# Performance work log

Hardware: AMD Instinct MI355X
Metric: run time of the kernel (lower is better)

The kernel has to match this reference:

```python
import jax, jax.numpy as jnp
import numpy as np

B, H, C, LB, PW = 8192, 128, 1, 64, 32
WL = LB + PW


def setup_inputs() -> dict:
    key = jax.random.key(0)
    ks = jax.random.split(key, 9)
    inv_sqrt_h = 1.0 / np.sqrt(H)
    return {
        "x": jax.random.normal(ks[0], (B, LB, 1), jnp.float32),
        # per-step Linear weights for F (hidden->hidden) and H (hidden->target)
        "F_w": jax.random.normal(ks[1], (WL, H, H), jnp.float32) * inv_sqrt_h,
        "F_b": jax.random.normal(ks[2], (WL, H), jnp.float32) * 0.05,
        "H_w": jax.random.normal(ks[3], (WL, C, H), jnp.float32) * inv_sqrt_h,
        "H_b": jax.random.normal(ks[4], (WL, C), jnp.float32) * 0.05,
        "init_state": jax.random.normal(ks[5], (H,), jnp.float32),
        # well-conditioned covariance / noise params so inv(S) is stable
        "init_cov": jnp.eye(H, dtype=jnp.float32) + 0.02 * jax.random.normal(ks[6], (H, H), jnp.float32),
        "Q": 0.1 * jnp.eye(H, dtype=jnp.float32) + 0.01 * jax.random.normal(ks[7], (H, H), jnp.float32),
        "R": 0.1 * jnp.eye(C, dtype=jnp.float32) + 0.01 * jax.random.normal(ks[8], (C, C), jnp.float32),
    }


def _kalman_forward(x, F_w, F_b, H_w, H_b, init_state, init_cov, Q, R):
    b = x.shape[0]
    h = init_state.shape[0]
    I = jnp.eye(h, dtype=x.dtype)
    hs0 = jnp.broadcast_to(init_state, (b, h))
    P0 = jnp.broadcast_to(init_cov, (b, h, h))
    obs = jnp.moveaxis(x[:, :LB, :C], 0, 1)  # (LB, B, C)

    def filt_step(carry, inp):
        hs, P = carry
        Fw, Fb, Hw, Hb, y = inp
        hs_pred = hs @ Fw.T + Fb                                   # (B, h)
        P_pred = jnp.einsum('ij,bjk,lk->bil', Fw, P, Fw) + Q       # (B, h, h)
        y_pred = hs_pred @ Hw.T + Hb                               # (B, c)
        resid = y - y_pred
        S = jnp.einsum('ij,bjk,lk->bil', Hw, P_pred, Hw) + R       # (B, c, c)
        PHt = jnp.einsum('bij,kj->bik', P_pred, Hw)                # (B, h, c)
        K = PHt @ jnp.linalg.inv(S)                                # (B, h, c)
        hs_new = hs_pred + jnp.einsum('bhc,bc->bh', K, resid)
        P_new = (I - jnp.einsum('bhc,ck->bhk', K, Hw)) @ P_pred
        return (hs_new, P_new), None

    (hs, _), _ = jax.lax.scan(
        filt_step, (hs0, P0), (F_w[:LB], F_b[:LB], H_w[:LB], H_b[:LB], obs))

    def pred_step(hs, inp):
        Fw, Fb, Hw, Hb = inp
        hs = hs @ Fw.T + Fb
        em = hs @ Hw.T + Hb                                        # (B, c)
        return hs, em

    _, ems = jax.lax.scan(pred_step, hs, (F_w[LB:], F_b[LB:], H_w[LB:], H_b[LB:]))
    # ems: (PW, B, C) -> torch.cat(dim=1) order -> (B, PW*C) -> unsqueeze(-1)
    out = jnp.moveaxis(ems, 0, 1).reshape(b, PW * C)
    return out[..., None]


def reference(x, F_w, F_b, H_w, H_b, init_state, init_cov, Q, R):
    return _kalman_forward(x, F_w, F_b, H_w, H_b, init_state, init_cov, Q, R)
```

## Files before the change

kernel.cpp:

```cpp
#include <hip/hip_runtime.h>

#define NB 8192
#define NH 128
#define NLB 64
#define NPW 32
#define MAGIC 1234567
#define SP 136

typedef __attribute__((ext_vector_type(8))) __bf16 bf16x8;
typedef __attribute__((ext_vector_type(4))) __bf16 bf16x4;
typedef __attribute__((ext_vector_type(4))) float f32x4;

__device__ __forceinline__ f32x4 mfma3(bf16x8 ah, bf16x8 al, bf16x8 bh, bf16x8 bl, f32x4 c) {
    c = __builtin_amdgcn_mfma_f32_16x16x32_bf16(ah, bh, c, 0, 0, 0);
    c = __builtin_amdgcn_mfma_f32_16x16x32_bf16(ah, bl, c, 0, 0, 0);
    c = __builtin_amdgcn_mfma_f32_16x16x32_bf16(al, bh, c, 0, 0, 0);
    return c;
}

__device__ __forceinline__ void ld_split8(const float* p, bf16x8& h, bf16x8& l) {
    float vv[8];
    *(float4*)vv       = *(const float4*)p;
    *(float4*)(vv + 4) = *(const float4*)(p + 4);
#pragma unroll
    for (int j = 0; j < 8; ++j) {
        __bf16 t = (__bf16)vv[j];
        h[j] = t;
        l[j] = (__bf16)(vv[j] - (float)t);
    }
}

#define KT_OFF   560
#define g63_OFF  (KT_OFF + 8192)
#define MR_OFF   (g63_OFF + 128)
#define DV_OFF   (MR_OFF + 2048)
#define DP_OFF   (DV_OFF + 32)
#define UV_OFF   (DP_OFF + 32)
#define SINK_OFF 32000
#define FLAG_I   34000
#define FHI_OFF  40960
#define FLO_OFF  (FHI_OFF + 524288)
#define WS_SPLIT_BYTES  ((size_t)(FLO_OFF + 524288) * 4)

#define DYN_LDS  ((144 + 144 + 128 + 128) * SP * 2)

__global__ __launch_bounds__(256)
void k0_split(const float* __restrict__ F, float* __restrict__ ws)
{
    size_t e = ((size_t)blockIdx.x * 256 + threadIdx.x) * 8;
    __bf16* fh = (__bf16*)(ws + FHI_OFF);
    __bf16* fl = (__bf16*)(ws + FLO_OFF);
    float v[8];
    *(float4*)v       = *(const float4*)(F + e);
    *(float4*)(v + 4) = *(const float4*)(F + e + 4);
    bf16x8 h, l;
#pragma unroll
    for (int j = 0; j < 8; ++j) {
        __bf16 t = (__bf16)v[j];
        h[j] = t;
        l[j] = (__bf16)(v[j] - (float)t);
    }
    *(bf16x8*)&fh[e] = h;
    *(bf16x8*)&fl[e] = l;
}

__global__ __launch_bounds__(1024) __attribute__((amdgpu_waves_per_eu(4, 4)))
void k1_recur(const float* __restrict__ Fw,
              const float* __restrict__ Fb,
              const float* __restrict__ Hw,
              const float* __restrict__ Hb,
              const float* __restrict__ init_state,
              const float* __restrict__ init_cov,
              const float* __restrict__ Qm,
              const float* __restrict__ Rm,
              float* __restrict__ ws,
              int use_split)
{
    const int tid = threadIdx.x;
    const int wg  = blockIdx.x;
    int* wsl = (int*)ws;

    extern __shared__ __align__(16) char dsm[];
    __bf16* PhiS = (__bf16*)dsm;
    __bf16* PloS = PhiS + 144 * SP;
    __bf16* UhiS = PloS + 144 * SP;
    __bf16* UloS = UhiS + 128 * SP;

    __shared__ float smisc[1280];
    __shared__ __align__(16) float shH[NH];
    __shared__ __align__(16) float shFW[NH];
    __shared__ float shK[NH], shV[NH], shFV[NH], shG[NH], shGn[NH];
    __shared__ float scal[16];

    float* pV = smisc;
    float* pW = smisc + 640;

    if (wg == 0) {
        const float Rv = Rm[0];
        const int lane = tid & 63, w = tid >> 6;
        const int lm = lane & 15, kg = lane >> 4;
        const int a = w >> 2, b = w & 3;
        const int arow = a * 32, bcol = b * 32;

#pragma unroll
        for (int ii = 0; ii < 16; ++ii) {
            int e = tid + ii * 1024;
            int r = e >> 7, c = e & 127;
            float v = init_cov[e];
            __bf16 h = (__bf16)v;
            PhiS[r * SP + c] = h;
            PloS[r * SP + c] = (__bf16)(v - (float)h);
        }
#pragma unroll
        for (int ii = 0; ii < 2; ++ii) {
            int e = tid + ii * 1024;
            int r = 128 + (e >> 7), c = e & 127;
            float v = (r == 130) ? init_state[c] : 0.f;
            __bf16 h = (__bf16)v;
            PhiS[r * SP + c] = h;
            PloS[r * SP + c] = (__bf16)(v - (float)h);
        }
        if (tid < NH) shG[tid] = init_state[tid];
        if (tid == 0) scal[1] = 0.f;

        f32x4 qreg[2][2];
#pragma unroll
        for (int rt2 = 0; rt2 < 2; ++rt2)
#pragma unroll
            for (int ct2 = 0; ct2 < 2; ++ct2)
                qreg[rt2][ct2] =
                    *(const f32x4*)&Qm[(bcol + rt2 * 16 + lm) * 128 + arow + ct2 * 16 + kg * 4];
        __syncthreads();

        for (int t = 0; t < NLB; ++t) {
            if (tid < NH) shH[tid] = Hw[t * NH + tid];
            bf16x8 fbH[2][4], fbL[2][4];
            if (use_split) {
                const __bf16* fh = (const __bf16*)(ws + FHI_OFF) + (size_t)t * 16384;
                const __bf16* fl = (const __bf16*)(ws + FLO_OFF) + (size_t)t * 16384;
#pragma unroll
                for (int rs = 0; rs < 2; ++rs)
#pragma unroll
                    for (int kc = 0; kc < 4; ++kc) {
                        int ro = (bcol + rs * 16 + lm) * 128 + kc * 32 + kg * 8;
                        fbH[rs][kc] = *(const bf16x8*)&fh[ro];
                        fbL[rs][kc] = *(const bf16x8*)&fl[ro];
                    }
            } else {
                const float* Ft = Fw + (size_t)t * 16384;
#pragma unroll
                for (int rs = 0; rs < 2; ++rs)
#pragma unroll
                    for (int kc = 0; kc < 4; ++kc)
                        ld_split8(Ft + (bcol + rs * 16 + lm) * 128 + kc * 32 + kg * 8,
                                  fbH[rs][kc], fbL[rs][kc]);
            }

            const f32x4 zero4 = {0.f, 0.f, 0.f, 0.f};
            f32x4 accU[2][2];
#pragma unroll
            for (int rt = 0; rt < 2; ++rt)
#pragma unroll
                for (int ct = 0; ct < 2; ++ct) accU[rt][ct] = zero4;
#pragma unroll
            for (int kc = 0; kc < 4; ++kc) {
#pragma unroll
                for (int rt = 0; rt < 2; ++rt) {
                    bf16x8 ph = *(bf16x8*)&PhiS[(arow + rt * 16 + lm) * SP + kc * 32 + kg * 8];
                    bf16x8 pl = *(bf16x8*)&PloS[(arow + rt * 16 + lm) * SP + kc * 32 + kg * 8];
#pragma unroll
                    for (int ct = 0; ct < 2; ++ct)
                        accU[rt][ct] = mfma3(ph, pl, fbH[ct][kc], fbL[ct][kc], accU[rt][ct]);
                }
            }
            if (a == 0) {
                f32x4 accV[2];
                accV[0] = zero4; accV[1] = zero4;
#pragma unroll
                for (int kc = 0; kc < 4; ++kc) {
                    bf16x8 vh = *(bf16x8*)&PhiS[(128 + lm) * SP + kc * 32 + kg * 8];
                    bf16x8 vl = *(bf16x8*)&PloS[(128 + lm) * SP + kc * 32 + kg * 8];
#pragma unroll
                    for (int ct = 0; ct < 2; ++ct)
                        accV[ct] = mfma3(vh, vl, fbH[ct][kc], fbL[ct][kc], accV[ct]);
                }
                if (kg == 0) {
#pragma unroll
                    for (int ct = 0; ct < 2; ++ct) {
                        int c = bcol + ct * 16 + lm;
                        shFW[c] = accV[ct][0];
                        shFV[c] = accV[ct][1];
                        shGn[c] = accV[ct][2];
                    }
                }
            }
#pragma unroll
            for (int rt = 0; rt < 2; ++rt)
#pragma unroll
                for (int ct = 0; ct < 2; ++ct) {
                    int Urow = arow + rt * 16 + kg * 4;
                    int Ucol = bcol + ct * 16 + lm;
                    bf16x4 uh, ul;
#pragma unroll
                    for (int reg = 0; reg < 4; ++reg) {
                        float v = accU[rt][ct][reg];
                        __bf16 h = (__bf16)v;
                        uh[reg] = h;
                        ul[reg] = (__bf16)(v - (float)h);
                    }
                    *(bf16x4*)&UhiS[Ucol * SP + Urow] = uh;
                    *(bf16x4*)&UloS[Ucol * SP + Urow] = ul;
                }
            __syncthreads();

            f32x4 accP[2][2];
#pragma unroll
            for (int rt2 = 0; rt2 < 2; ++rt2)
#pragma unroll
                for (int ct2 = 0; ct2 < 2; ++ct2) accP[rt2][ct2] = qreg[rt2][ct2];
#pragma unroll
            for (int kc = 0; kc < 4; ++kc) {
#pragma unroll
                for (int ct2 = 0; ct2 < 2; ++ct2) {
                    bf16x8 uh = *(bf16x8*)&UhiS[(arow + ct2 * 16 + lm) * SP + kc * 32 + kg * 8];
                    bf16x8 ul = *(bf16x8*)&UloS[(arow + ct2 * 16 + lm) * SP + kc * 32 + kg * 8];
#pragma unroll
                    for (int rt2 = 0; rt2 < 2; ++rt2)
                        accP[rt2][ct2] = mfma3(uh, ul, fbH[rt2][kc], fbL[rt2][kc], accP[rt2][ct2]);
                }
            }
            {
                float vr[2] = {0.f, 0.f};
                float wc[2][4];
#pragma unroll
                for (int i = 0; i < 2; ++i)
#pragma unroll
                    for (int j = 0; j < 4; ++j) wc[i][j] = 0.f;
#pragma unroll
                for (int rt2 = 0; rt2 < 2; ++rt2) {
                    int R = bcol + rt2 * 16 + lm;
                    float fvr = shFV[R];
                    float hr  = shH[R];
#pragma unroll
                    for (int ct2 = 0; ct2 < 2; ++ct2) {
                        int cb = arow + ct2 * 16 + kg * 4;
                        f32x4 fw4 = *(const f32x4*)&shFW[cb];
                        f32x4 h4  = *(const f32x4*)&shH[cb];
                        bf16x4 ph4, pl4;
#pragma unroll
                        for (int reg = 0; reg < 4; ++reg) {
                            float val = accP[rt2][ct2][reg] - fvr * fw4[reg];
                            __bf16 vh = (__bf16)val;
                            ph4[reg] = vh;
                            pl4[reg] = (__bf16)(val - (float)vh);
                            vr[rt2]      += val * h4[reg];
                            wc[ct2][reg] += val * hr;
                        }
                        *(bf16x4*)&PhiS[R * SP + cb] = ph4;
                        *(bf16x4*)&PloS[R * SP + cb] = pl4;
                    }
                }
#pragma unroll
                for (int rt2 = 0; rt2 < 2; ++rt2) {
                    vr[rt2] += __shfl_xor(vr[rt2], 16);
                    vr[rt2] += __shfl_xor(vr[rt2], 32);
                }
                if (kg == 0)
#pragma unroll
                    for (int rt2 = 0; rt2 < 2; ++rt2)
                        pV[(bcol + rt2 * 16 + lm) * 5 + a] = vr[rt2];
#pragma unroll
                for (int ct2 = 0; ct2 < 2; ++ct2)
#pragma unroll
                    for (int reg = 0; reg < 4; ++reg) {
#pragma unroll
                        for (int off = 1; off < 16; off <<= 1)
                            wc[ct2][reg] += __shfl_xor(wc[ct2][reg], off);
                    }
                if (lm == 0)
#pragma unroll
                    for (int ct2 = 0; ct2 < 2; ++ct2)
#pragma unroll
                        for (int reg = 0; reg < 4; ++reg)
                            pW[(arow + ct2 * 16 + kg * 4 + reg) * 5 + b] = wc[ct2][reg];
            }
            if (tid < NH) {
                float g = shGn[tid] + shFV[tid] * scal[1] + Fb[t * NH + tid];
                shG[tid] = g;
                __bf16 h = (__bf16)g;
                PhiS[130 * SP + tid] = h;
                PloS[130 * SP + tid] = (__bf16)(g - (float)h);
            }
            __syncthreads();

            if (tid < 64) {
                int j0 = tid, j1 = tid + 64;
                float v0 = pV[j0 * 5] + pV[j0 * 5 + 1] + pV[j0 * 5 + 2] + pV[j0 * 5 + 3];
                float v1 = pV[j1 * 5] + pV[j1 * 5 + 1] + pV[j1 * 5 + 2] + pV[j1 * 5 + 3];
                float p = shH[j0] * v0 + shH[j1] * v1;
#pragma unroll
                for (int off = 1; off < 64; off <<= 1) p += __shfl_xor(p, off);
                float s = 1.f / (Rv + p);
                float k0 = v0 * s, k1v = v1 * s;
                shK[j0] = k0; shK[j1] = k1v;
                ws[KT_OFF + t * 128 + j0] = k0;
                ws[KT_OFF + t * 128 + j1] = k1v;
                __bf16 h0 = (__bf16)k0;
                PhiS[129 * SP + j0] = h0;
                PloS[129 * SP + j0] = (__bf16)(k0 - (float)h0);
                __bf16 h1 = (__bf16)k1v;
                PhiS[129 * SP + j1] = h1;
                PloS[129 * SP + j1] = (__bf16)(k1v - (float)h1);
            } else if (tid < 128) {
                int c0 = tid - 64, c1 = tid;
                float w0 = pW[c0 * 5] + pW[c0 * 5 + 1] + pW[c0 * 5 + 2] + pW[c0 * 5 + 3];
                float w1 = pW[c1 * 5] + pW[c1 * 5 + 1] + pW[c1 * 5 + 2] + pW[c1 * 5 + 3];
                __bf16 h0 = (__bf16)w0;
                PhiS[128 * SP + c0] = h0;
                PloS[128 * SP + c0] = (__bf16)(w0 - (float)h0);
                __bf16 h1 = (__bf16)w1;
                PhiS[128 * SP + c1] = h1;
                PloS[128 * SP + c1] = (__bf16)(w1 - (float)h1);
            } else if (tid < 192) {
                int l = tid - 128;
                float p = shH[l] * shG[l] + shH[l + 64] * shG[l + 64];
#pragma unroll
                for (int off = 1; off < 64; off <<= 1) p += __shfl_xor(p, off);
                if (l == 0) scal[1] = -(p + Hb[t]);
            }
            __syncthreads();
        }

        if (tid < 128) ws[g63_OFF + tid] = shG[tid] + shK[tid] * scal[1];
        __syncthreads();
        if (tid == 0) {
            __threadfence();
            __atomic_store_n(&wsl[FLAG_I + 0], MAGIC, __ATOMIC_RELEASE);
        }
        return;
    }

    if (wg <= 32) {
        const int pt = 63 + wg;
        float* part = smisc;
        float* shU  = shV;
        if (tid < NH) shU[tid] = Hw[pt * NH + tid];
        if (tid == 0) scal[2] = Hb[pt];
        __syncthreads();

        for (int j = pt; j >= NLB; --j) {
            const float* Fj  = Fw + (size_t)j * 16384;
            const float* fbj = Fb + j * NH;
            if (tid < 64) {
                float a = shU[tid] * fbj[tid] + shU[tid + 64] * fbj[tid + 64];
#pragma unroll
                for (int off = 32; off; off >>= 1) a += __shfl_down(a, off);
                if (tid == 0) scal[2] += a;
            }
            {
                const int c = tid & 127, sgc = tid >> 7;
                float a = 0.f;
                const float* base = Fj + (size_t)(sgc * 16) * 128 + c;
#pragma unroll 4
                for (int i = 0; i < 16; ++i) a += shU[sgc * 16 + i] * base[(size_t)i * 128];
                part[c * 9 + sgc] = a;
            }
            __syncthreads();
            if (tid < 128) {
                float a = 0.f;
#pragma unroll
                for (int s = 0; s < 8; ++s) a += part[tid * 9 + s];
                shU[tid] = a;
            }
            __syncthreads();
        }

        if (tid < NH) ws[UV_OFF + (wg - 1) * NH + tid] = shU[tid];
        if (tid == 0) ws[DP_OFF + (wg - 1)] = scal[2];
        __syncthreads();
        if (tid == 0) {
            __threadfence();
            __atomic_store_n(&wsl[FLAG_I + wg * 16], MAGIC, __ATOMIC_RELEASE);
        }
        return;
    }

    {
        if (tid >= 256) return;
        const int lane = tid & 63;
        float r0 = 1.f + (float)tid * 1e-6f + (float)wg * 1e-5f;
        int rounds = 0;
        while (true) {
#pragma unroll 8
            for (int i = 0; i < 1024; ++i) r0 = __builtin_fmaf(r0, 0.99999988f, 1.0e-7f);
            int done = 0;
            if (lane == 0) {
                int cnt = 0;
                for (int w2 = 0; w2 <= 32; ++w2)
                    cnt += (__atomic_load_n(&wsl[FLAG_I + w2 * 16], __ATOMIC_RELAXED) == MAGIC);
                done = (cnt == 33) ? 1 : 0;
            }
            done = __shfl(done, 0);
            if (done || ++rounds > 4096) break;
        }
        if (r0 == 123.4567f) ws[SINK_OFF + wg] = r0;
    }
}

__global__ __launch_bounds__(256)
void k2_cols(const float* __restrict__ Fw,
             const float* __restrict__ Hw,
             float* __restrict__ ws)
{
    const int tid = threadIdx.x;
    const int c   = blockIdx.x;
    __shared__ float shX[128], shY[128], p2[256], pu[32 * 9];
    __shared__ float sc[1];

    if (c == 64) {
        int p = tid >> 3, sg = tid & 7;
        float a = 0.f;
#pragma unroll
        for (int i = 0; i < 16; ++i)
            a += ws[UV_OFF + p * 128 + sg * 16 + i] * ws[g63_OFF + sg * 16 + i];
        pu[p * 9 + sg] = a;
        __syncthreads();
        if (tid < 32) {
            float d = ws[DP_OFF + tid];
#pragma unroll
            for (int s = 0; s < 8; ++s) d += pu[tid * 9 + s];
            ws[DV_OFF + tid] = d;
        }
        return;
    }

    if (tid < 128) shX[tid] = ws[KT_OFF + c * 128 + tid];
    __syncthreads();

    for (int j = c + 1; j < NLB; ++j) {
        const float* Fj = Fw + (size_t)j * 16384;
        {
            int r = tid & 127, sg = tid >> 7;
            float a = 0.f;
            const float4* fr = (const float4*)(Fj + r * 128 + sg * 64);
#pragma unroll
            for (int q = 0; q < 16; ++q) {
                float4 f = fr[q];
                int m = sg * 64 + q * 4;
                a += f.x * shX[m] + f.y * shX[m+1] + f.z * shX[m+2] + f.w * shX[m+3];
            }
            p2[sg * 128 + r] = a;
        }
        __syncthreads();
        if (tid < 128) shY[tid] = p2[tid] + p2[128 + tid];
        __syncthreads();
        if (tid < 64) {
            float a = Hw[j * 128 + 2*tid] * shY[2*tid] + Hw[j * 128 + 2*tid + 1] * shY[2*tid + 1];
#pragma unroll
            for (int off = 32; off; off >>= 1) a += __shfl_down(a, off);
            if (tid == 0) sc[0] = a;
        }
        __syncthreads();
        if (tid < 128) shX[tid] = shY[tid] - ws[KT_OFF + j * 128 + tid] * sc[0];
        __syncthreads();
    }

    {
        int p = tid >> 3, sg = tid & 7;
        float a = 0.f;
#pragma unroll
        for (int i = 0; i < 16; ++i)
            a += ws[UV_OFF + p * 128 + sg * 16 + i] * shX[sg * 16 + i];
        pu[p * 9 + sg] = a;
        __syncthreads();
        if (tid < 32) {
            float a = 0.f;
#pragma unroll
            for (int s = 0; s < 8; ++s) a += pu[tid * 9 + s];
            ws[MR_OFF + tid * 64 + c] = a;
        }
    }
}

__global__ __launch_bounds__(1024)
void k3_batch(const float* __restrict__ x,
              const float* __restrict__ ws,
              float* __restrict__ out)
{
    const int tid = threadIdx.x;
    const int wgb = blockIdx.x;
    __shared__ float Ml[NPW * 65];
    __shared__ float dl[NPW];

#pragma unroll
    for (int ii = 0; ii < 2; ++ii) {
        int idx = tid + ii * 1024;
        int p = idx >> 6, n = idx & 63;
        Ml[p * 65 + n] = ws[MR_OFF + p * 64 + n];
    }
    if (tid < NPW) dl[tid] = ws[DV_OFF + tid];
    __syncthreads();

    const int r  = wgb * 256 + (tid >> 2);
    const int pg = tid & 3;
    float acc[8];
#pragma unroll
    for (int pi = 0; pi < 8; ++pi) acc[pi] = dl[pg * 8 + pi];
    const float4* xr = (const float4*)(x + (size_t)r * 64);
#pragma unroll
    for (int c4 = 0; c4 < 16; ++c4) {
        float4 xv = xr[c4];
#pragma unroll
        for (int pi = 0; pi < 8; ++pi) {
            const float* mrow = &Ml[(pg * 8 + pi) * 65 + c4 * 4];
            acc[pi] += xv.x * mrow[0] + xv.y * mrow[1] + xv.z * mrow[2] + xv.w * mrow[3];
        }
    }
    float* op = out + (size_t)r * 32 + pg * 8;
    *(float4*)op       = make_float4(acc[0], acc[1], acc[2], acc[3]);
    *(float4*)(op + 4) = make_float4(acc[4], acc[5], acc[6], acc[7]);
}

extern "C" void kernel_launch(void* const* d_in, const int* in_sizes, int n_in,
                              void* d_out, int out_size, void* d_ws, size_t ws_size,
                              hipStream_t stream) {
    const float* x          = (const float*)d_in[0];
    const float* F_w        = (const float*)d_in[1];
    const float* F_b        = (const float*)d_in[2];
    const float* H_w        = (const float*)d_in[3];
    const float* H_b        = (const float*)d_in[4];
    const float* init_state = (const float*)d_in[5];
    const float* init_cov   = (const float*)d_in[6];
    const float* Qm         = (const float*)d_in[7];
    const float* Rm         = (const float*)d_in[8];
    float* ws   = (float*)d_ws;
    float* outp = (float*)d_out;

    int use_split = (ws_size >= WS_SPLIT_BYTES + 65536) ? 1 : 0;

    (void)hipFuncSetAttribute((const void*)k1_recur,
                              hipFuncAttributeMaxDynamicSharedMemorySize, DYN_LDS);

    if (use_split)
        k0_split<<<dim3(512), dim3(256), 0, stream>>>(F_w, ws);
    k1_recur<<<dim3(256), dim3(1024), DYN_LDS, stream>>>(
        F_w, F_b, H_w, H_b, init_state, init_cov, Qm, Rm, ws, use_split);
    k2_cols<<<dim3(65), dim3(256), 0, stream>>>(F_w, H_w, ws);
    k3_batch<<<dim3(32), dim3(1024), 0, stream>>>(x, ws, outp);
}
```

Baseline: 1.167 ms.

## Defer Kalman gain/reduction phase into next step, overlapping with F loads

Restructures the serial filter loop in workgroup 0. The end-of-step phase (gain, W-vector and scalar residual reductions) now runs at the start of the next iteration, while that step's F weights are loading. H rows are double-buffered in shared memory and the next F_b is prefetched into a register. The V-row MFMA is moved after the P update, an extra barrier is added mid-step, and s_setprio is raised around the MFMA blocks. Net barrier count per step is unchanged, but the dependency chain is reordered and shK is no longer written during the loop (only in the final epilogue).

```diff
diff --git a/kernel.cpp b/kernel.cpp
--- a/kernel.cpp
+++ b/kernel.cpp
@@ -87,7 +87,7 @@
     __bf16* UloS = UhiS + 128 * SP;
 
     __shared__ float smisc[1280];
-    __shared__ __align__(16) float shH[NH];
+    __shared__ __align__(16) float shHb[2][NH];
     __shared__ __align__(16) float shFW[NH];
     __shared__ float shK[NH], shV[NH], shFV[NH], shG[NH], shGn[NH];
     __shared__ float scal[16];
@@ -130,10 +130,16 @@
             for (int ct2 = 0; ct2 < 2; ++ct2)
                 qreg[rt2][ct2] =
                     *(const f32x4*)&Qm[(bcol + rt2 * 16 + lm) * 128 + arow + ct2 * 16 + kg * 4];
+
+        float hbp = 0.f;
         __syncthreads();
 
         for (int t = 0; t < NLB; ++t) {
-            if (tid < NH) shH[tid] = Hw[t * NH + tid];
+            float fbv = 0.f;
+            if (tid < NH) {
+                shHb[t & 1][tid] = Hw[t * NH + tid];
+                fbv = Fb[t * NH + tid];
+            }
             bf16x8 fbH[2][4], fbL[2][4];
             if (use_split) {
                 const __bf16* fh = (const __bf16*)(ws + FHI_OFF) + (size_t)t * 16384;
@@ -156,12 +162,52 @@
                                   fbH[rs][kc], fbL[rs][kc]);
             }
 
+            if (t > 0) {
+                const float* hp = shHb[(t - 1) & 1];
+                if (tid < 64) {
+                    int j0 = tid, j1 = tid + 64;
+                    float v0 = pV[j0 * 5] + pV[j0 * 5 + 1] + pV[j0 * 5 + 2] + pV[j0 * 5 + 3];
+                    float v1 = pV[j1 * 5] + pV[j1 * 5 + 1] + pV[j1 * 5 + 2] + pV[j1 * 5 + 3];
+                    float p = hp[j0] * v0 + hp[j1] * v1;
+#pragma unroll
+                    for (int off = 1; off < 64; off <<= 1) p += __shfl_xor(p, off);
+                    float s = 1.f / (Rv + p);
+                    float k0 = v0 * s, k1v = v1 * s;
+                    ws[KT_OFF + (t - 1) * 128 + j0] = k0;
+                    ws[KT_OFF + (t - 1) * 128 + j1] = k1v;
+                    __bf16 h0 = (__bf16)k0;
+                    PhiS[129 * SP + j0] = h0;
+                    PloS[129 * SP + j0] = (__bf16)(k0 - (float)h0);
+                    __bf16 h1 = (__bf16)k1v;
+                    PhiS[129 * SP + j1] = h1;
+                    PloS[129 * SP + j1] = (__bf16)(k1v - (float)h1);
+                } else if (tid < 128) {
+                    int c0 = tid - 64, c1 = tid;
+                    float w0 = pW[c0 * 5] + pW[c0 * 5 + 1] + pW[c0 * 5 + 2] + pW[c0 * 5 + 3];
+                    float w1 = pW[c1 * 5] + pW[c1 * 5 + 1] + pW[c1 * 5 + 2] + pW[c1 * 5 + 3];
+                    __bf16 h0 = (__bf16)w0;
+                    PhiS[128 * SP + c0] = h0;
+                    PloS[128 * SP + c0] = (__bf16)(w0 - (float)h0);
+                    __bf16 h1 = (__bf16)w1;
+                    PhiS[128 * SP + c1] = h1;
+                    PloS[128 * SP + c1] = (__bf16)(w1 - (float)h1);
+                } else if (tid < 192) {
+                    int l = tid - 128;
+                    float p = hp[l] * shG[l] + hp[l + 64] * shG[l + 64];
+#pragma unroll
+                    for (int off = 1; off < 64; off <<= 1) p += __shfl_xor(p, off);
+                    if (l == 0) scal[1] = -(p + hbp);
+                }
+            }
+            if (tid >= 128 && tid < 192) hbp = Hb[t];
+
             const f32x4 zero4 = {0.f, 0.f, 0.f, 0.f};
             f32x4 accU[2][2];
 #pragma unroll
             for (int rt = 0; rt < 2; ++rt)
 #pragma unroll
                 for (int ct = 0; ct < 2; ++ct) accU[rt][ct] = zero4;
+            __builtin_amdgcn_s_setprio(1);
 #pragma unroll
             for (int kc = 0; kc < 4; ++kc) {
 #pragma unroll
@@ -173,27 +219,7 @@
                         accU[rt][ct] = mfma3(ph, pl, fbH[ct][kc], fbL[ct][kc], accU[rt][ct]);
                 }
             }
-            if (a == 0) {
-                f32x4 accV[2];
-                accV[0] = zero4; accV[1] = zero4;
-#pragma unroll
-                for (int kc = 0; kc < 4; ++kc) {
-                    bf16x8 vh = *(bf16x8*)&PhiS[(128 + lm) * SP + kc * 32 + kg * 8];
-                    bf16x8 vl = *(bf16x8*)&PloS[(128 + lm) * SP + kc * 32 + kg * 8];
-#pragma unroll
-                    for (int ct = 0; ct < 2; ++ct)
-                        accV[ct] = mfma3(vh, vl, fbH[ct][kc], fbL[ct][kc], accV[ct]);
-                }
-                if (kg == 0) {
-#pragma unroll
-                    for (int ct = 0; ct < 2; ++ct) {
-                        int c = bcol + ct * 16 + lm;
-                        shFW[c] = accV[ct][0];
-                        shFV[c] = accV[ct][1];
-                        shGn[c] = accV[ct][2];
-                    }
-                }
-            }
+            __builtin_amdgcn_s_setprio(0);
 #pragma unroll
             for (int rt = 0; rt < 2; ++rt)
 #pragma unroll
@@ -218,6 +244,7 @@
             for (int rt2 = 0; rt2 < 2; ++rt2)
 #pragma unroll
                 for (int ct2 = 0; ct2 < 2; ++ct2) accP[rt2][ct2] = qreg[rt2][ct2];
+            __builtin_amdgcn_s_setprio(1);
 #pragma unroll
             for (int kc = 0; kc < 4; ++kc) {
 #pragma unroll
@@ -229,7 +256,32 @@
                         accP[rt2][ct2] = mfma3(uh, ul, fbH[rt2][kc], fbL[rt2][kc], accP[rt2][ct2]);
                 }
             }
+            __builtin_amdgcn_s_setprio(0);
+            if (a == 0) {
+                f32x4 accV[2];
+                accV[0] = zero4; accV[1] = zero4;
+#pragma unroll
+                for (int kc = 0; kc < 4; ++kc) {
+                    bf16x8 vh = *(bf16x8*)&PhiS[(128 + lm) * SP + kc * 32 + kg * 8];
+                    bf16x8 vl = *(bf16x8*)&PloS[(128 + lm) * SP + kc * 32 + kg * 8];
+#pragma unroll
+                    for (int ct = 0; ct < 2; ++ct)
+                        accV[ct] = mfma3(vh, vl, fbH[ct][kc], fbL[ct][kc], accV[ct]);
+                }
+                if (kg == 0) {
+#pragma unroll
+                    for (int ct = 0; ct < 2; ++ct) {
+                        int c = bcol + ct * 16 + lm;
+                        shFW[c] = accV[ct][0];
+                        shFV[c] = accV[ct][1];
+                        shGn[c] = accV[ct][2];
+                    }
+                }
+            }
+            __syncthreads();
+
             {
+                const float* hcur = shHb[t & 1];
                 float vr[2] = {0.f, 0.f};
                 float wc[2][4];
 #pragma unroll
@@ -240,12 +292,12 @@
                 for (int rt2 = 0; rt2 < 2; ++rt2) {
                     int R = bcol + rt2 * 16 + lm;
                     float fvr = shFV[R];
-                    float hr  = shH[R];
+                    float hr  = hcur[R];
 #pragma unroll
                     for (int ct2 = 0; ct2 < 2; ++ct2) {
                         int cb = arow + ct2 * 16 + kg * 4;
                         f32x4 fw4 = *(const f32x4*)&shFW[cb];
-                        f32x4 h4  = *(const f32x4*)&shH[cb];
+                        f32x4 h4  = *(const f32x4*)&hcur[cb];
                         bf16x4 ph4, pl4;
 #pragma unroll
                         for (int reg = 0; reg < 4; ++reg) {
@@ -285,52 +337,38 @@
                             pW[(arow + ct2 * 16 + kg * 4 + reg) * 5 + b] = wc[ct2][reg];
             }
             if (tid < NH) {
-                float g = shGn[tid] + shFV[tid] * scal[1] + Fb[t * NH + tid];
+                float g = shGn[tid] + shFV[tid] * scal[1] + fbv;
                 shG[tid] = g;
                 __bf16 h = (__bf16)g;
                 PhiS[130 * SP + tid] = h;
                 PloS[130 * SP + tid] = (__bf16)(g - (float)h);
             }
             __syncthreads();
-
+        }
+
+        {
+            const float* hp = shHb[1];
             if (tid < 64) {
                 int j0 = tid, j1 = tid + 64;
                 float v0 = pV[j0 * 5] + pV[j0 * 5 + 1] + pV[j0 * 5 + 2] + pV[j0 * 5 + 3];
                 float v1 = pV[j1 * 5] + pV[j1 * 5 + 1] + pV[j1 * 5 + 2] + pV[j1 * 5 + 3];
-                float p = shH[j0] * v0 + shH[j1] * v1;
+                float p = hp[j0] * v0 + hp[j1] * v1;
 #pragma unroll
                 for (int off = 1; off < 64; off <<= 1) p += __shfl_xor(p, off);
                 float s = 1.f / (Rv + p);
                 float k0 = v0 * s, k1v = v1 * s;
                 shK[j0] = k0; shK[j1] = k1v;
-                ws[KT_OFF + t * 128 + j0] = k0;
-                ws[KT_OFF + t * 128 + j1] = k1v;
-                __bf16 h0 = (__bf16)k0;
-                PhiS[129 * SP + j0] = h0;
-                PloS[129 * SP + j0] = (__bf16)(k0 - (float)h0);
-                __bf16 h1 = (__bf16)k1v;
-                PhiS[129 * SP + j1] = h1;
-                PloS[129 * SP + j1] = (__bf16)(k1v - (float)h1);
-            } else if (tid < 128) {
-                int c0 = tid - 64, c1 = tid;
-                float w0 = pW[c0 * 5] + pW[c0 * 5 + 1] + pW[c0 * 5 + 2] + pW[c0 * 5 + 3];
-                float w1 = pW[c1 * 5] + pW[c1 * 5 + 1] + pW[c1 * 5 + 2] + pW[c1 * 5 + 3];
-                __bf16 h0 = (__bf16)w0;
-                PhiS[128 * SP + c0] = h0;
-                PloS[128 * SP + c0] = (__bf16)(w0 - (float)h0);
-                __bf16 h1 = (__bf16)w1;
-                PhiS[128 * SP + c1] = h1;
-                PloS[128 * SP + c1] = (__bf16)(w1 - (float)h1);
-            } else if (tid < 192) {
+                ws[KT_OFF + 63 * 128 + j0] = k0;
+                ws[KT_OFF + 63 * 128 + j1] = k1v;
+            } else if (tid >= 128 && tid < 192) {
                 int l = tid - 128;
-                float p = shH[l] * shG[l] + shH[l + 64] * shG[l + 64];
+                float p = hp[l] * shG[l] + hp[l + 64] * shG[l + 64];
 #pragma unroll
                 for (int off = 1; off < 64; off <<= 1) p += __shfl_xor(p, off);
-                if (l == 0) scal[1] = -(p + Hb[t]);
-            }
-            __syncthreads();
-        }
-
+                if (l == 0) scal[1] = -(p + hbp);
+            }
+        }
+        __syncthreads();
         if (tid < 128) ws[g63_OFF + tid] = shG[tid] + shK[tid] * scal[1];
         __syncthreads();
         if (tid == 0) {
```

Result: slower. 1.236 ms (+5.9%).

## Overlap column propagation with the filter recurrence via per-step flags

Applied to the files above, without the earlier changes.

The separate k2_cols kernel is removed. Its 64 column-propagation workloads now run inside k1_recur as workgroups 33..96, which spin on per-timestep release flags published by the recurrence workgroup and consume each gain vector as soon as it is written. The final U·X projection and the DV computation move into k3_batch, and the old idle-spinner completion check now waits on a single final flag. This hides the serial column chain behind the main recurrence and drops one launch, but it relies on all workgroups being co-resident and on spin-waiting, which competes for GPU resources.

```diff
diff --git a/kernel.cpp b/kernel.cpp
--- a/kernel.cpp
+++ b/kernel.cpp
@@ -36,8 +36,10 @@
 #define DV_OFF   (MR_OFF + 2048)
 #define DP_OFF   (DV_OFF + 32)
 #define UV_OFF   (DP_OFF + 32)
+#define XC_OFF   16000
 #define SINK_OFF 32000
 #define FLAG_I   34000
+#define SFLAG_I  (FLAG_I + 1600)
 #define FHI_OFF  40960
 #define FLO_OFF  (FHI_OFF + 524288)
 #define WS_SPLIT_BYTES  ((size_t)(FLO_OFF + 524288) * 4)
@@ -87,6 +89,7 @@
     __bf16* UloS = UhiS + 128 * SP;
 
     __shared__ float smisc[1280];
+    __shared__ __align__(16) float shHb[2][NH];
     __shared__ __align__(16) float shH[NH];
     __shared__ __align__(16) float shFW[NH];
     __shared__ float shK[NH], shV[NH], shFV[NH], shG[NH], shGn[NH];
@@ -133,6 +136,10 @@
         __syncthreads();
 
         for (int t = 0; t < NLB; ++t) {
+            if (t && tid == 512)
+                __hip_atomic_store(&wsl[SFLAG_I + (t - 1) * 16], MAGIC,
+                                   __ATOMIC_RELEASE, __HIP_MEMORY_SCOPE_AGENT);
+
             if (tid < NH) shH[tid] = Hw[t * NH + tid];
             bf16x8 fbH[2][4], fbL[2][4];
             if (use_split) {
@@ -303,8 +310,10 @@
                 float s = 1.f / (Rv + p);
                 float k0 = v0 * s, k1v = v1 * s;
                 shK[j0] = k0; shK[j1] = k1v;
-                ws[KT_OFF + t * 128 + j0] = k0;
-                ws[KT_OFF + t * 128 + j1] = k1v;
+                __hip_atomic_store(&ws[KT_OFF + t * 128 + j0], k0,
+                                   __ATOMIC_RELAXED, __HIP_MEMORY_SCOPE_AGENT);
+                __hip_atomic_store(&ws[KT_OFF + t * 128 + j1], k1v,
+                                   __ATOMIC_RELAXED, __HIP_MEMORY_SCOPE_AGENT);
                 __bf16 h0 = (__bf16)k0;
                 PhiS[129 * SP + j0] = h0;
                 PloS[129 * SP + j0] = (__bf16)(k0 - (float)h0);
@@ -331,12 +340,10 @@
             __syncthreads();
         }
 
+        if (tid == 512)
+            __hip_atomic_store(&wsl[SFLAG_I + 63 * 16], MAGIC,
+                               __ATOMIC_RELEASE, __HIP_MEMORY_SCOPE_AGENT);
         if (tid < 128) ws[g63_OFF + tid] = shG[tid] + shK[tid] * scal[1];
-        __syncthreads();
-        if (tid == 0) {
-            __threadfence();
-            __atomic_store_n(&wsl[FLAG_I + 0], MAGIC, __ATOMIC_RELEASE);
-        }
         return;
     }
 
@@ -377,11 +384,76 @@
 
         if (tid < NH) ws[UV_OFF + (wg - 1) * NH + tid] = shU[tid];
         if (tid == 0) ws[DP_OFF + (wg - 1)] = scal[2];
+        return;
+    }
+
+    if (wg <= 96) {
+        const int c = wg - 33;
+        float* p2  = (float*)dsm;
+        float* shX = shHb[0];
+        float* shY = shHb[1];
+
+        if (tid == 0) {
+            int spins = 0;
+            while (__hip_atomic_load(&wsl[SFLAG_I + c * 16],
+                                     __ATOMIC_ACQUIRE, __HIP_MEMORY_SCOPE_AGENT) != MAGIC) {
+                __builtin_amdgcn_s_sleep(4);
+                if (++spins > (1 << 25)) break;
+            }
+        }
         __syncthreads();
-        if (tid == 0) {
-            __threadfence();
-            __atomic_store_n(&wsl[FLAG_I + wg * 16], MAGIC, __ATOMIC_RELEASE);
-        }
+        if (tid < 128)
+            shX[tid] = __hip_atomic_load(&ws[KT_OFF + c * 128 + tid],
+                                         __ATOMIC_RELAXED, __HIP_MEMORY_SCOPE_AGENT);
+        __syncthreads();
+
+        for (int j = c + 1; j < NLB; ++j) {
+            const float* Fj = Fw + (size_t)j * 16384;
+            {
+                int r = tid & 127, sg = tid >> 7;
+                float a = 0.f;
+                const float4* fr = (const float4*)(Fj + r * 128 + sg * 16);
+#pragma unroll
+                for (int q = 0; q < 4; ++q) {
+                    float4 f = fr[q];
+                    int m = sg * 16 + q * 4;
+                    a += f.x * shX[m] + f.y * shX[m+1] + f.z * shX[m+2] + f.w * shX[m+3];
+                }
+                p2[sg * 128 + r] = a;
+            }
+            __syncthreads();
+            if (tid < 128) {
+                float y = 0.f;
+#pragma unroll
+                for (int s = 0; s < 8; ++s) y += p2[s * 128 + tid];
+                shY[tid] = y;
+            }
+            __syncthreads();
+            if (tid < 64) {
+                float a = Hw[j * 128 + 2*tid] * shY[2*tid] + Hw[j * 128 + 2*tid + 1] * shY[2*tid + 1];
+#pragma unroll
+                for (int off = 32; off; off >>= 1) a += __shfl_down(a, off);
+                if (tid == 0) scal[0] = a;
+            }
+            __syncthreads();
+            if (tid == 0) {
+                int spins = 0;
+                while (__hip_atomic_load(&wsl[SFLAG_I + j * 16],
+                                         __ATOMIC_ACQUIRE, __HIP_MEMORY_SCOPE_AGENT) != MAGIC) {
+                    __builtin_amdgcn_s_sleep(4);
+                    if (++spins > (1 << 25)) break;
+                }
+            }
+            __syncthreads();
+            if (tid < 128) {
+                float ktj = __hip_atomic_load(&ws[KT_OFF + j * 128 + tid],
+                                              __ATOMIC_RELAXED, __HIP_MEMORY_SCOPE_AGENT);
+                shX[tid] = shY[tid] - ktj * scal[0];
+            }
+            __syncthreads();
+        }
+
+        if (tid < 128) ws[XC_OFF + c * 128 + tid] = shX[tid];
         return;
     }
 
@@ -394,91 +466,13 @@
 #pragma unroll 8
             for (int i = 0; i < 1024; ++i) r0 = __builtin_fmaf(r0, 0.99999988f, 1.0e-7f);
             int done = 0;
-            if (lane == 0) {
-                int cnt = 0;
-                for (int w2 = 0; w2 <= 32; ++w2)
-                    cnt += (__atomic_load_n(&wsl[FLAG_I + w2 * 16], __ATOMIC_RELAXED) == MAGIC);
-                done = (cnt == 33) ? 1 : 0;
-            }
+            if (lane == 0)
+                done = (__hip_atomic_load(&wsl[SFLAG_I + 63 * 16],
+                                          __ATOMIC_RELAXED, __HIP_MEMORY_SCOPE_AGENT) == MAGIC);
             done = __shfl(done, 0);
-            if (done || ++rounds > 4096) break;
+            if (done || ++rounds > 8192) break;
         }
         if (r0 == 123.4567f) ws[SINK_OFF + wg] = r0;
-    }
-}
-
-__global__ __launch_bounds__(256)
-void k2_cols(const float* __restrict__ Fw,
-             const float* __restrict__ Hw,
-             float* __restrict__ ws)
-{
-    const int tid = threadIdx.x;
-    const int c   = blockIdx.x;
-    __shared__ float shX[128], shY[128], p2[256], pu[32 * 9];
-    __shared__ float sc[1];
-
-    if (c == 64) {
-        int p = tid >> 3, sg = tid & 7;
-        float a = 0.f;
-#pragma unroll
-        for (int i = 0; i < 16; ++i)
-            a += ws[UV_OFF + p * 128 + sg * 16 + i] * ws[g63_OFF + sg * 16 + i];
-        pu[p * 9 + sg] = a;
-        __syncthreads();
-        if (tid < 32) {
-            float d = ws[DP_OFF + tid];
-#pragma unroll
-            for (int s = 0; s < 8; ++s) d += pu[tid * 9 + s];
-            ws[DV_OFF + tid] = d;
-        }
-        return;
-    }
-
-    if (tid < 128) shX[tid] = ws[KT_OFF + c * 128 + tid];
-    __syncthreads();
-
-    for (int j = c + 1; j < NLB; ++j) {
-        const float* Fj = Fw + (size_t)j * 16384;
-        {
-            int r = tid & 127, sg = tid >> 7;
-            float a = 0.f;
-            const float4* fr = (const float4*)(Fj + r * 128 + sg * 64);
-#pragma unroll
-            for (int q = 0; q < 16; ++q) {
-                float4 f = fr[q];
-                int m = sg * 64 + q * 4;
-                a += f.x * shX[m] + f.y * shX[m+1] + f.z * shX[m+2] + f.w * shX[m+3];
-            }
-            p2[sg * 128 + r] = a;
-        }
-        __syncthreads();
-        if (tid < 128) shY[tid] = p2[tid] + p2[128 + tid];
-        __syncthreads();
-        if (tid < 64) {
-            float a = Hw[j * 128 + 2*tid] * shY[2*tid] + Hw[j * 128 + 2*tid + 1] * shY[2*tid + 1];
-#pragma unroll
-            for (int off = 32; off; off >>= 1) a += __shfl_down(a, off);
-            if (tid == 0) sc[0] = a;
-        }
-        __syncthreads();
-        if (tid < 128) shX[tid] = shY[tid] - ws[KT_OFF + j * 128 + tid] * sc[0];
-        __syncthreads();
-    }
-
-    {
-        int p = tid >> 3, sg = tid & 7;
-        float a = 0.f;
-#pragma unroll
-        for (int i = 0; i < 16; ++i)
-            a += ws[UV_OFF + p * 128 + sg * 16 + i] * shX[sg * 16 + i];
-        pu[p * 9 + sg] = a;
-        __syncthreads();
-        if (tid < 32) {
-            float a = 0.f;
-#pragma unroll
-            for (int s = 0; s < 8; ++s) a += pu[tid * 9 + s];
-            ws[MR_OFF + tid * 64 + c] = a;
-        }
     }
 }
 
@@ -492,13 +486,32 @@
     __shared__ float Ml[NPW * 65];
     __shared__ float dl[NPW];
 
-#pragma unroll
-    for (int ii = 0; ii < 2; ++ii) {
-        int idx = tid + ii * 1024;
-        int p = idx >> 6, n = idx & 63;
-        Ml[p * 65 + n] = ws[MR_OFF + p * 64 + n];
-    }
-    if (tid < NPW) dl[tid] = ws[DV_OFF + tid];
+    {
+        int p = tid >> 5, l = tid & 31;
+        float a = 0.f;
+#pragma unroll
+        for (int q = 0; q < 4; ++q)
+            a += ws[UV_OFF + p * 128 + l + q * 32] * ws[g63_OFF + l + q * 32];
+#pragma unroll
+        for (int off = 1; off < 32; off <<= 1) a += __shfl_xor(a, off);
+        if (l == 0) dl[p] = ws[DP_OFF + p] + a;
+    }
+    {
+        int p0 = tid >> 6, n = tid & 63;
+        const float4* xc = (const float4*)&ws[XC_OFF + n * 128];
+#pragma unroll
+        for (int pp = 0; pp < 2; ++pp) {
+            int p = p0 + pp * 16;
+            const float4* up = (const float4*)&ws[UV_OFF + p * 128];
+            float a = 0.f;
+#pragma unroll
+            for (int q = 0; q < 32; ++q) {
+                float4 u4 = up[q]; float4 c4 = xc[q];
+                a += u4.x * c4.x + u4.y * c4.y + u4.z * c4.z + u4.w * c4.w;
+            }
+            Ml[p * 65 + n] = a;
+        }
+    }
     __syncthreads();
 
     const int r  = wgb * 256 + (tid >> 2);
@@ -545,6 +558,5 @@
         k0_split<<<dim3(512), dim3(256), 0, stream>>>(F_w, ws);
     k1_recur<<<dim3(256), dim3(1024), DYN_LDS, stream>>>(
         F_w, F_b, H_w, H_b, init_state, init_cov, Qm, Rm, ws, use_split);
-    k2_cols<<<dim3(65), dim3(256), 0, stream>>>(F_w, H_w, ws);
     k3_batch<<<dim3(32), dim3(1024), 0, stream>>>(x, ws, outp);
 }
```

New measurement: 1.834 ms. 57.2% more time.
